# Kernel optimization log

Measured on AMD Instinct MI355X. Metric: run time of the kernel, lower is better.

## Reference

```python
import jax, jax.numpy as jnp
import numpy as np

EPS = 1e-5  # torch BatchNorm2d default eps


def _lin(x, W, b):
    # torch nn.Linear: y = x @ W.T + b, W is [out, in]
    return jnp.einsum('...i,oi->...o', x, W) + b


def _bn(x, g, b):
    # BatchNorm2d in training mode: normalize per channel (last axis here)
    # over all other axes (B, N, K) with biased variance.
    m = jnp.mean(x, axis=(0, 1, 2), keepdims=True)
    v = jnp.mean(jnp.square(x - m), axis=(0, 1, 2), keepdims=True)
    return (x - m) * jax.lax.rsqrt(v + EPS) * g + b


def _gelu(x):
    return jax.nn.gelu(x, approximate=False)  # torch F.gelu default is erf


def _knn_idx(points, k):
    # squared euclidean pairwise distances, then k smallest per query
    pn = jnp.sum(points * points, axis=-1)  # [B,N]
    d2 = pn[:, :, None] + pn[:, None, :] - 2.0 * jnp.einsum('bnd,bmd->bnm', points, points)
    _, idx = jax.lax.top_k(-d2, k)  # [B,N,k], nearest first (includes self)
    return idx


def _gather(x, idx):
    # x: [B,N,D], idx: [B,N,K] -> [B,N,K,D]
    return jax.vmap(lambda a, i: a[i])(x, idx)


def setup_inputs() -> dict:
    key = jax.random.key(0)
    ks = jax.random.split(key, 20)
    B, N, Dp, Df, k = 2, 8192, 3, 128, 16

    def lin_params(kw, kb, din, dout):
        s = 1.0 / np.sqrt(din)
        W = jax.random.uniform(kw, (dout, din), jnp.float32, -s, s)
        b = jax.random.uniform(kb, (dout,), jnp.float32, -s, s)
        return W, b

    Wq, bq = lin_params(ks[0], ks[1], Df, Df)
    Wk, bk = lin_params(ks[2], ks[3], Df, Df)
    Wv, bv = lin_params(ks[4], ks[5], Df, Df)
    Wd1, bd1 = lin_params(ks[6], ks[7], Dp, Dp)
    Wd2, bd2 = lin_params(ks[8], ks[9], Dp, Df)
    Wg1, bg1 = lin_params(ks[10], ks[11], Df, Df)
    Wg2, bg2 = lin_params(ks[12], ks[13], Df, Df)

    return {
        'feats': jax.random.normal(ks[14], (B, N, Df), jnp.float32),
        'points': jax.random.normal(ks[15], (B, N, Dp), jnp.float32),
        'Wq': Wq, 'bq': bq, 'Wk': Wk, 'bk': bk, 'Wv': Wv, 'bv': bv,
        'Wd1': Wd1, 'bd1': bd1, 'Wd2': Wd2, 'bd2': bd2,
        'Wg1': Wg1, 'bg1': bg1, 'Wg2': Wg2, 'bg2': bg2,
        'gd': jnp.ones((Dp,), jnp.float32), 'betad': jnp.zeros((Dp,), jnp.float32),
        'gg1': jnp.ones((Df,), jnp.float32), 'betag1': jnp.zeros((Df,), jnp.float32),
        'gg2': jnp.ones((Df,), jnp.float32), 'betag2': jnp.zeros((Df,), jnp.float32),
        'k': 16,
    }


def reference(feats, points, Wq, bq, Wk, bk, Wv, bv, Wd1, bd1, Wd2, bd2,
              Wg1, bg1, Wg2, bg2, gd, betad, gg1, betag1, gg2, betag2, k):
    idx = _knn_idx(points, k)                     # [B,N,k]
    knn_feats = _gather(feats, idx)               # [B,N,k,Df]
    knn_points = _gather(points, idx)             # [B,N,k,Dp]

    pos = points[:, :, None, :] - knn_points      # [B,N,k,Dp]
    pos = _lin(pos, Wd1, bd1)
    pos = _gelu(_bn(pos, gd, betad))
    pos = _lin(pos, Wd2, bd2)                     # [B,N,k,Df]

    q = _lin(feats, Wq, bq)                       # [B,N,Df]
    key_t = _lin(knn_feats, Wk, bk)               # [B,N,k,Df]
    gamma = q[:, :, None, :] - key_t + pos
    gamma = _gelu(_bn(gamma, gg1, betag1))
    gamma = _lin(gamma, Wg1, bg1)
    gamma = _gelu(_bn(gamma, gg2, betag2))
    gamma = _lin(gamma, Wg2, bg2)

    rho = jax.nn.softmax(gamma, axis=-2)          # softmax over k neighbors
    value = _lin(knn_feats, Wv, bv) + pos
    return jnp.einsum('bnkd,bnkd->bnd', rho, value)
```

## Files before the change

kernel.cpp:

```cpp
#include <hip/hip_runtime.h>
#include <hip/hip_bf16.h>
#include <math.h>

#define NPTS 8192
#define STAT_CNT 262144.0f
#define BN_EPS 1e-5f

typedef __attribute__((__ext_vector_type__(8))) __bf16 bf16x8;
typedef __attribute__((__ext_vector_type__(4))) float f32x4;

#define SD_SUM 0
#define SD_SSQ 4
#define SD_SC 8
#define SD_SH 12
#define SG1_SC 16
#define SG1_SH 144
#define SG2_SC 272
#define SG2_SH 400
#define PG1 528
#define PG2 8720
#define STATS_FLOATS 16912

__device__ __forceinline__ unsigned short f2b(float x){
  unsigned u = __float_as_uint(x);
  return (unsigned short)((u + 0x7FFFu + ((u>>16)&1u)) >> 16);
}
__device__ __forceinline__ float b2f(unsigned short h){
  return __uint_as_float(((unsigned)h)<<16);
}
__device__ __forceinline__ float gelu_f(float x){
  float u = fabsf(x)*0.70710678118654752440f;
  float t = 1.0f/fmaf(0.3275911f, u, 1.0f);
  float p = t*fmaf(t,fmaf(t,fmaf(t,fmaf(t,1.061405429f,-1.453152027f),1.421413741f),-0.284496736f),0.254829592f);
  float er = fmaf(-p, __expf(-u*u), 1.0f);
  er = (x < 0.f) ? -er : er;
  return 0.5f*x*(1.0f+er);
}
__device__ __forceinline__ int swz(int row, int byteInRow){
  return row*256 + (byteInRow ^ ((row&7)<<4));
}
__device__ __forceinline__ float dist2f(float qx,float qy,float qz,float qpn,
                                        float x,float y,float z,float w){
  return (qpn + w) - 2.0f*fmaf(qx,x,fmaf(qy,y,qz*z));
}

#define MFMA16(a,b,c) __builtin_amdgcn_mfma_f32_16x16x32_bf16((a),(b),(c),0,0,0)

__device__ __forceinline__ bf16x8 ldsA8(const unsigned short* sA, int row, int k){
  return *(const bf16x8*)((const char*)sA + swz(row, k*2));
}
__device__ __forceinline__ bf16x8 ldW8(const unsigned short* W, int n, int k){
  return *(const bf16x8*)(W + n*128 + k);
}

__device__ __forceinline__ bf16x8 bn_gelu8(uint4 raw, const float* sSC, const float* sSH, int kb0){
  union { f32x4 v[2]; float f[8]; } SC, SH;
  SC.v[0] = *(const f32x4*)&sSC[kb0]; SC.v[1] = *(const f32x4*)&sSC[kb0+4];
  SH.v[0] = *(const f32x4*)&sSH[kb0]; SH.v[1] = *(const f32x4*)&sSH[kb0+4];
  union { uint4 u; unsigned int w[4]; } U; U.u = raw;
  union { unsigned int w[4]; bf16x8 v; } O;
  #pragma unroll
  for (int p=0;p<4;++p){
    float xlo = gelu_f(fmaf(__uint_as_float(U.w[p]<<16),        SC.f[2*p],   SH.f[2*p]));
    float xhi = gelu_f(fmaf(__uint_as_float(U.w[p]&0xffff0000u), SC.f[2*p+1], SH.f[2*p+1]));
    unsigned lo = __float_as_uint(xlo), hi = __float_as_uint(xhi);
    lo = (lo + 0x7FFFu + ((lo>>16)&1u)) >> 16;
    hi = (hi + 0x7FFFu + ((hi>>16)&1u)) & 0xffff0000u;
    O.w[p] = hi | lo;
  }
  return O.v;
}

__global__ __launch_bounds__(256) void k_prep(
    const float* __restrict__ feats, const float* __restrict__ Wq, const float* __restrict__ Wk,
    const float* __restrict__ Wv, const float* __restrict__ Wg1, const float* __restrict__ Wg2,
    unsigned short* __restrict__ wbf, unsigned short* __restrict__ featb, float* __restrict__ stats)
{
  int i = blockIdx.x*256 + threadIdx.x;
  featb[i] = f2b(feats[i]);
  if (i < 16384){
    wbf[i]        = f2b(Wq[i]);
    wbf[16384+i]  = f2b(Wk[i]);
    wbf[32768+i]  = f2b(Wv[i]);
    wbf[49152+i]  = f2b(Wg1[i]);
    wbf[65536+i]  = f2b(Wg2[i]);
  }
  if (i < STATS_FLOATS) stats[i] = 0.f;
}

__global__ __launch_bounds__(256) void k_knn5(const float* __restrict__ points, int* __restrict__ idxb){
  __shared__ float svD[16][64];
  __shared__ int   svI[16][64];
  __shared__ int   svC[16];
  int tid = threadIdx.x;
  int wid = tid>>6, lane = tid&63;
  int blk = blockIdx.x;
  int b = (blk*16) >> 13;
  const float* cb = points + (size_t)b*NPTS*3;
  int qbase = blk*16 + wid*4;
  float qx[4],qy[4],qz[4],qpn[4],lmin[4],tq[4];
  #pragma unroll
  for (int q=0;q<4;++q){
    const float* qp = points + (size_t)(qbase+q)*3;
    qx[q]=qp[0]; qy[q]=qp[1]; qz[q]=qp[2];
    qpn[q]=fmaf(qz[q],qz[q],fmaf(qy[q],qy[q],qx[q]*qx[q]));
    lmin[q]=3.4e38f;
  }
  if (lane < 4) svC[wid*4+lane] = 0;
  #pragma unroll 4
  for (int s=0;s<128;++s){
    int p = s*64 + lane;
    const float* sp = cb + (size_t)p*3;
    float x=sp[0], y=sp[1], z=sp[2];
    float w = fmaf(z,z,fmaf(y,y,x*x));
    #pragma unroll
    for (int q=0;q<4;++q){
      float d = dist2f(qx[q],qy[q],qz[q],qpn[q], x,y,z,w);
      lmin[q] = fminf(lmin[q], d);
    }
  }
  #pragma unroll
  for (int q=0;q<4;++q){
    float v = lmin[q];
    #pragma unroll
    for (int k=2;k<=64;k<<=1){
      #pragma unroll
      for (int j=k>>1;j>=1;j>>=1){
        float o = __shfl_xor(v, j);
        bool keepmin = ((lane & j)==0) == ((lane & k)==0);
        v = keepmin ? fminf(v,o) : fmaxf(v,o);
      }
    }
    tq[q] = __shfl(v, 15);
  }
  #pragma unroll 2
  for (int s=0;s<128;++s){
    int p = s*64 + lane;
    const float* sp = cb + (size_t)p*3;
    float x=sp[0], y=sp[1], z=sp[2];
    float w = fmaf(z,z,fmaf(y,y,x*x));
    #pragma unroll
    for (int q=0;q<4;++q){
      float d = dist2f(qx[q],qy[q],qz[q],qpn[q], x,y,z,w);
      if (d <= tq[q]){
        int wq = wid*4+q;
        int slot = atomicAdd(&svC[wq], 1);
        if (slot < 64){ svD[wq][slot]=d; svI[wq][slot]=p; }
      }
    }
  }
  __syncthreads();
  #pragma unroll 1
  for (int q=0;q<4;++q){
    int wq = wid*4+q;
    int n = svC[wq]; n = (n>64)?64:n;
    float d = (lane<n)? svD[wq][lane] : 3.4e38f;
    int   ii = (lane<n)? svI[wq][lane] : 0x7fffffff;
    int rank = 0;
    #pragma unroll 4
    for (int j=0;j<n;++j){
      float od = svD[wq][j]; int oi = svI[wq][j];
      rank += ((od<d)||(od==d && oi<ii)) ? 1 : 0;
    }
    if (lane<n && rank<16) idxb[(size_t)(qbase+q)*16 + rank] = ii;
  }
}

__global__ __launch_bounds__(256) void k_dstats(const int* __restrict__ idxb,
    const float* __restrict__ points, const float* __restrict__ Wd1, const float* __restrict__ bd1,
    float* __restrict__ stats){
  __shared__ float sS[6];
  if (threadIdx.x < 6) sS[threadIdx.x]=0.f;
  __syncthreads();
  int qi = blockIdx.x*256 + threadIdx.x;
  int b = qi >> 13;
  const float* qp = points + (size_t)qi*3;
  float qx=qp[0],qy=qp[1],qz=qp[2];
  float w00=Wd1[0],w01=Wd1[1],w02=Wd1[2],w10=Wd1[3],w11=Wd1[4],w12=Wd1[5],w20=Wd1[6],w21=Wd1[7],w22=Wd1[8];
  float b0=bd1[0],b1=bd1[1],b2=bd1[2];
  float s0=0,s1=0,s2=0,q0=0,q1=0,q2=0;
  #pragma unroll
  for (int j=0;j<16;j++){
    int nb = idxb[(size_t)qi*16 + j];
    const float* np_ = points + (size_t)(b*NPTS + nb)*3;
    float dx=qx-np_[0], dy=qy-np_[1], dz=qz-np_[2];
    float t0 = fmaf(dz,w02,fmaf(dy,w01,dx*w00)) + b0;
    float t1 = fmaf(dz,w12,fmaf(dy,w11,dx*w10)) + b1;
    float t2 = fmaf(dz,w22,fmaf(dy,w21,dx*w20)) + b2;
    s0+=t0; s1+=t1; s2+=t2;
    q0=fmaf(t0,t0,q0); q1=fmaf(t1,t1,q1); q2=fmaf(t2,t2,q2);
  }
  atomicAdd(&sS[0],s0); atomicAdd(&sS[1],s1); atomicAdd(&sS[2],s2);
  atomicAdd(&sS[3],q0); atomicAdd(&sS[4],q1); atomicAdd(&sS[5],q2);
  __syncthreads();
  if (threadIdx.x < 3) atomicAdd(&stats[SD_SUM+threadIdx.x], sS[threadIdx.x]);
  else if (threadIdx.x < 6) atomicAdd(&stats[SD_SSQ+threadIdx.x-3], sS[threadIdx.x]);
}

__global__ void k_finalize(float* stats, int sumOff, int ssqOff, const float* __restrict__ gm,
                           const float* __restrict__ bt, int scOff, int shOff, int C){
  int c = blockIdx.x*64 + threadIdx.x;
  if (c >= C) return;
  float m = stats[sumOff+c] * (1.0f/STAT_CNT);
  float v = stats[ssqOff+c] * (1.0f/STAT_CNT) - m*m;
  v = fmaxf(v, 0.0f);
  float rs = rsqrtf(v + BN_EPS);
  float sc = gm[c]*rs;
  stats[scOff+c] = sc;
  stats[shOff+c] = fmaf(-m, sc, bt[c]);
}

__global__ void k_finalizeP(float* stats, int partOff, const float* __restrict__ gm,
                            const float* __restrict__ bt, int scOff, int shOff){
  int c = blockIdx.x*64 + threadIdx.x;
  float s=0.f, q=0.f;
  #pragma unroll 4
  for (int p=0;p<32;p++){
    s += stats[partOff + p*256 + c];
    q += stats[partOff + p*256 + 128 + c];
  }
  float m = s * (1.0f/STAT_CNT);
  float v = fmaxf(q*(1.0f/STAT_CNT) - m*m, 0.0f);
  float rs = rsqrtf(v + BN_EPS);
  float sc = gm[c]*rs;
  stats[scOff+c] = sc;
  stats[shOff+c] = fmaf(-m, sc, bt[c]);
}

__global__ __launch_bounds__(256) void k_qkv(
    const unsigned short* __restrict__ featb, const unsigned short* __restrict__ wbf,
    const float* __restrict__ bq, const float* __restrict__ bk, const float* __restrict__ bv,
    float* __restrict__ qout, unsigned short* __restrict__ kout, unsigned short* __restrict__ vout)
{
  __shared__ __align__(16) unsigned short sA[64*128];
  int tid = threadIdx.x;
  size_t row0g = (size_t)blockIdx.x*64;
  for (int t=tid; t<1024; t+=256){
    int row=t>>4, cc=t&15;
    uint4 v = *(const uint4*)(featb + (row0g+row)*128 + cc*8);
    *(uint4*)((char*)sA + swz(row, cc*16)) = v;
  }
  __syncthreads();
  int wid=tid>>6, lane=tid&63;
  int r=lane&15, g=lane>>4;
  int row0 = wid*16;
  f32x4 aQ[8]={}, aK[8]={}, aV[8]={};
  const unsigned short* WQ = wbf;
  const unsigned short* WK = wbf+16384;
  const unsigned short* WV = wbf+32768;
  #pragma unroll
  for (int ks=0;ks<4;++ks){
    int k = ks*32 + g*8;
    bf16x8 a0 = ldsA8(sA, row0+r, k);
    #pragma unroll
    for (int nt=0;nt<8;++nt){
      aQ[nt]=MFMA16(a0, ldW8(WQ,nt*16+r,k), aQ[nt]);
      aK[nt]=MFMA16(a0, ldW8(WK,nt*16+r,k), aK[nt]);
      aV[nt]=MFMA16(a0, ldW8(WV,nt*16+r,k), aV[nt]);
    }
  }
  #pragma unroll
  for (int nt=0;nt<8;++nt){
    int ch=nt*16+r;
    float bqc=bq[ch], bkc=bk[ch], bvc=bv[ch];
    #pragma unroll
    for (int rr=0;rr<4;++rr){
      size_t grow = row0g + row0 + g*4 + rr;
      qout[grow*128+ch] = aQ[nt][rr]+bqc;
      kout[grow*128+ch] = f2b(aK[nt][rr]+bkc);
      vout[grow*128+ch] = f2b(aV[nt][rr]+bvc);
    }
  }
}

__global__ __launch_bounds__(256) void k_fuse(
    const float* __restrict__ points, const int* __restrict__ idxb,
    const float* __restrict__ qbuf, const unsigned short* __restrict__ kb,
    const unsigned short* __restrict__ vb,
    const float* __restrict__ Wd1, const float* __restrict__ bd1,
    const float* __restrict__ Wd2, const float* __restrict__ bd2,
    float* __restrict__ stats,
    unsigned short* __restrict__ g1out, unsigned short* __restrict__ valout)
{
  __shared__ float sSum[128];
  __shared__ float sSq[128];
  int tid = threadIdx.x, blk = blockIdx.x;
  int slot = tid & 15, jg = tid >> 4;
  int lane = tid & 63;
  int ch0 = slot*8;
  if (tid < 128){ sSum[tid]=0.f; sSq[tid]=0.f; }
  float w2[24], b2v[8];
  #pragma unroll
  for (int u=0;u<8;++u){
    w2[u*3+0]=Wd2[(ch0+u)*3+0];
    w2[u*3+1]=Wd2[(ch0+u)*3+1];
    w2[u*3+2]=Wd2[(ch0+u)*3+2];
    b2v[u]=bd2[ch0+u];
  }
  int c = slot & 3; c = (c==3)?2:c;
  float wa  = (c==0)?Wd1[0]:((c==1)?Wd1[3]:Wd1[6]);
  float wb_ = (c==0)?Wd1[1]:((c==1)?Wd1[4]:Wd1[7]);
  float wc  = (c==0)?Wd1[2]:((c==1)?Wd1[5]:Wd1[8]);
  float bc_ = (c==0)?bd1[0]:((c==1)?bd1[1]:bd1[2]);
  float sc_ = (c==0)?stats[SD_SC+0]:((c==1)?stats[SD_SC+1]:stats[SD_SC+2]);
  float sh_ = (c==0)?stats[SD_SH+0]:((c==1)?stats[SD_SH+1]:stats[SD_SH+2]);
  int base = lane & 48;
  float accS[8]={0,0,0,0,0,0,0,0}, accQ[8]={0,0,0,0,0,0,0,0};
  __syncthreads();
  #pragma unroll 2
  for (int i=0;i<8;++i){
    int q = blk*8 + i;
    int b = q >> 13;
    int row = q*16 + jg;
    int nb = idxb[row];
    const float* ctr = points + (size_t)q*3;
    const float* np_ = points + (size_t)(b*NPTS + nb)*3;
    float dx = ctr[0]-np_[0], dy = ctr[1]-np_[1], dz = ctr[2]-np_[2];
    float t = fmaf(dz, wc, fmaf(dy, wb_, dx*wa)) + bc_;
    float tc = gelu_f(fmaf(t, sc_, sh_));
    float g0  = __shfl(tc, base+0);
    float g1v = __shfl(tc, base+1);
    float g2v = __shfl(tc, base+2);
    size_t kvoff = ((size_t)(b*NPTS + nb))*128 + ch0;
    union { uint4 u; unsigned short s[8]; } K, V, G, Vo;
    K.u = *(const uint4*)(kb + kvoff);
    V.u = *(const uint4*)(vb + kvoff);
    float4 q0 = *(const float4*)(qbuf + (size_t)q*128 + ch0);
    float4 q1 = *(const float4*)(qbuf + (size_t)q*128 + ch0 + 4);
    float qv[8] = {q0.x,q0.y,q0.z,q0.w,q1.x,q1.y,q1.z,q1.w};
    #pragma unroll
    for (int u=0;u<8;++u){
      float pos = fmaf(g2v, w2[u*3+2], fmaf(g1v, w2[u*3+1], g0*w2[u*3+0])) + b2v[u];
      float key = b2f(K.s[u]);
      float val = b2f(V.s[u]) + pos;
      float gmv = qv[u] - key + pos;
      accS[u] += gmv; accQ[u] = fmaf(gmv,gmv,accQ[u]);
      G.s[u] = f2b(gmv); Vo.s[u] = f2b(val);
    }
    *(uint4*)(g1out + (size_t)row*128 + ch0) = G.u;
    *(uint4*)(valout + (size_t)row*128 + ch0) = Vo.u;
  }
  #pragma unroll
  for (int u=0;u<8;++u){
    atomicAdd(&sSum[ch0+u], accS[u]);
    atomicAdd(&sSq[ch0+u], accQ[u]);
  }
  __syncthreads();
  if (tid < 128){
    int ps = blk & 31;
    atomicAdd(&stats[PG1 + ps*256 + tid], sSum[tid]);
    atomicAdd(&stats[PG1 + ps*256 + 128 + tid], sSq[tid]);
  }
}

__global__ __launch_bounds__(512) void k_g(
    const unsigned short* __restrict__ gin, const unsigned short* __restrict__ W,
    const float* __restrict__ bias, float* __restrict__ stats, int scOff, int shOff,
    unsigned short* __restrict__ gout, int partOff)
{
  __shared__ __align__(16) unsigned short sW[128*128];
  __shared__ float sSC[128], sSH[128];
  int tid = threadIdx.x;
  for (int t=tid; t<2048; t+=512){
    int row=t>>4, c=t&15;
    uint4 v = *(const uint4*)(W + row*128 + c*8);
    *(uint4*)((char*)sW + swz(row,c*16)) = v;
  }
  if (tid < 128){ sSC[tid]=stats[scOff+tid]; sSH[tid]=stats[shOff+tid]; }
  __syncthreads();
  int wid=tid>>6, lane=tid&63;
  int r=lane&15, g=lane>>4;
  float bs[8];
  #pragma unroll
  for (int nt=0;nt<8;++nt) bs[nt]=bias[nt*16+r];
  float accS[8]={0,0,0,0,0,0,0,0}, accQ[8]={0,0,0,0,0,0,0,0};
  for (int tile = blockIdx.x*8 + wid; tile < 16384; tile += 8192){
    size_t row0 = (size_t)tile*16;
    bf16x8 a[4];
    #pragma unroll
    for (int ks=0;ks<4;++ks){
      int kb0 = ks*32 + g*8;
      uint4 raw = *(const uint4*)(gin + (row0+r)*128 + kb0);
      a[ks] = bn_gelu8(raw, sSC, sSH, kb0);
    }
    f32x4 acc[8] = {};
    #pragma unroll
    for (int ks=0;ks<4;++ks){
      int k = ks*32 + g*8;
      #pragma unroll
      for (int nt=0;nt<8;++nt)
        acc[nt] = MFMA16(a[ks], ldsA8(sW, nt*16+r, k), acc[nt]);
    }
    #pragma unroll
    for (int nt=0;nt<8;++nt){
      #pragma unroll
      for (int rr=0;rr<4;++rr){
        float x = acc[nt][rr] + bs[nt];
        accS[nt] += x; accQ[nt] = fmaf(x,x,accQ[nt]);
        gout[(row0 + g*4 + rr)*128 + nt*16 + r] = f2b(x);
      }
    }
  }
  #pragma unroll
  for (int nt=0;nt<8;++nt){
    float s_ = accS[nt], q_ = accQ[nt];
    s_ += __shfl_xor(s_,16); s_ += __shfl_xor(s_,32);
    q_ += __shfl_xor(q_,16); q_ += __shfl_xor(q_,32);
    if (g==0){
      int slot = blockIdx.x & 31;
      atomicAdd(&stats[partOff + slot*256 + nt*16+r], s_);
      atomicAdd(&stats[partOff + slot*256 + 128 + nt*16+r], q_);
    }
  }
}

__global__ __launch_bounds__(512) void k_out(
    const unsigned short* __restrict__ gin, const unsigned short* __restrict__ W,
    const float* __restrict__ bias, const float* __restrict__ stats, int scOff, int shOff,
    const unsigned short* __restrict__ val, float* __restrict__ outp)
{
  __shared__ __align__(16) unsigned short sW[128*128];
  __shared__ float sSC[128], sSH[128];
  int tid = threadIdx.x;
  for (int t=tid; t<2048; t+=512){
    int row=t>>4, c=t&15;
    uint4 v = *(const uint4*)(W + row*128 + c*8);
    *(uint4*)((char*)sW + swz(row,c*16)) = v;
  }
  if (tid < 128){ sSC[tid]=stats[scOff+tid]; sSH[tid]=stats[shOff+tid]; }
  __syncthreads();
  int wid=tid>>6, lane=tid&63;
  int r=lane&15, g=lane>>4;
  float bs[8];
  #pragma unroll
  for (int nt=0;nt<8;++nt) bs[nt]=bias[nt*16+r];
  for (int tile = blockIdx.x*8 + wid; tile < 16384; tile += 8192){
    size_t row0 = (size_t)tile*16;
    bf16x8 a[4];
    #pragma unroll
    for (int ks=0;ks<4;++ks){
      int kb0 = ks*32 + g*8;
      uint4 raw = *(const uint4*)(gin + (row0+r)*128 + kb0);
      a[ks] = bn_gelu8(raw, sSC, sSH, kb0);
    }
    f32x4 acc[8] = {};
    #pragma unroll
    for (int ks=0;ks<4;++ks){
      int k = ks*32 + g*8;
      #pragma unroll
      for (int nt=0;nt<8;++nt)
        acc[nt] = MFMA16(a[ks], ldsA8(sW, nt*16+r, k), acc[nt]);
    }
    #pragma unroll
    for (int nt=0;nt<8;++nt){
      float g3[4];
      #pragma unroll
      for (int rr=0;rr<4;++rr) g3[rr] = acc[nt][rr] + bs[nt];
      float m = fmaxf(fmaxf(g3[0],g3[1]),fmaxf(g3[2],g3[3]));
      m = fmaxf(m, __shfl_xor(m,16));
      m = fmaxf(m, __shfl_xor(m,32));
      float s=0.f, o=0.f;
      #pragma unroll
      for (int rr=0;rr<4;++rr){
        float e = __expf(g3[rr]-m);
        float vv = b2f(val[(row0 + g*4 + rr)*128 + nt*16 + r]);
        s += e; o = fmaf(e, vv, o);
      }
      s += __shfl_xor(s,16); s += __shfl_xor(s,32);
      o += __shfl_xor(o,16); o += __shfl_xor(o,32);
      if (g==0) outp[(size_t)tile*128 + nt*16 + r] = o/s;
    }
  }
}

extern "C" void kernel_launch(void* const* d_in, const int* in_sizes, int n_in,
                              void* d_out, int out_size, void* d_ws, size_t ws_size,
                              hipStream_t stream)
{
  const float* feats  = (const float*)d_in[0];
  const float* points = (const float*)d_in[1];
  const float* Wq = (const float*)d_in[2];  const float* bq = (const float*)d_in[3];
  const float* Wk = (const float*)d_in[4];  const float* bk = (const float*)d_in[5];
  const float* Wv = (const float*)d_in[6];  const float* bv = (const float*)d_in[7];
  const float* Wd1= (const float*)d_in[8];  const float* bd1= (const float*)d_in[9];
  const float* Wd2= (const float*)d_in[10]; const float* bd2= (const float*)d_in[11];
  const float* Wg1= (const float*)d_in[12]; const float* bg1= (const float*)d_in[13];
  const float* Wg2= (const float*)d_in[14]; const float* bg2= (const float*)d_in[15];
  const float* gd = (const float*)d_in[16]; const float* betad = (const float*)d_in[17];
  const float* gg1= (const float*)d_in[18]; const float* betag1= (const float*)d_in[19];
  const float* gg2= (const float*)d_in[20]; const float* betag2= (const float*)d_in[21];
  float* outp = (float*)d_out;

  char* ws = (char*)d_ws;
  int*    idxb  = (int*)   (ws + 0);
  float*  stats = (float*) (ws + 1048576);
  unsigned short* wbf   = (unsigned short*)(ws + 1179648);
  unsigned short* featb = (unsigned short*)(ws + 1343488);
  unsigned short* kb    = (unsigned short*)(ws + 5537792);
  unsigned short* vbuf  = (unsigned short*)(ws + 9732096);
  unsigned short* g1b = (unsigned short*)(ws + 13926400);
  unsigned short* vab = (unsigned short*)(ws + 81035264);
  unsigned short* g2b = (unsigned short*)(ws + 148144128);
  float*  qbuf  = (float*) (ws + 215252992);

  k_prep<<<dim3(8192),dim3(256),0,stream>>>(feats,Wq,Wk,Wv,Wg1,Wg2,wbf,featb,stats);
  k_knn5<<<dim3(1024),dim3(256),0,stream>>>(points,idxb);
  k_dstats<<<dim3(64),dim3(256),0,stream>>>(idxb,points,Wd1,bd1,stats);
  k_finalize<<<dim3(1),dim3(64),0,stream>>>(stats,SD_SUM,SD_SSQ,gd,betad,SD_SC,SD_SH,3);
  k_qkv<<<dim3(256),dim3(256),0,stream>>>(featb,wbf,bq,bk,bv,qbuf,kb,vbuf);
  k_fuse<<<dim3(2048),dim3(256),0,stream>>>(points,idxb,qbuf,kb,vbuf,Wd1,bd1,Wd2,bd2,stats,g1b,vab);
  k_finalizeP<<<dim3(2),dim3(64),0,stream>>>(stats,PG1,gg1,betag1,SG1_SC,SG1_SH);
  k_g<<<dim3(1024),dim3(512),0,stream>>>(g1b,wbf+49152,bg1,stats,SG1_SC,SG1_SH,g2b,PG2);
  k_finalizeP<<<dim3(2),dim3(64),0,stream>>>(stats,PG2,gg2,betag2,SG2_SC,SG2_SH);
  k_out<<<dim3(1024),dim3(512),0,stream>>>(g2b,wbf+65536,bg2,stats,SG2_SC,SG2_SH,vab,outp);
  (void)in_sizes; (void)n_in; (void)out_size; (void)ws_size;
}
```

Before: 348.5 us.

## Stage k_g and k_out global traffic through LDS for coalesced 16-byte accesses

In k_g, the per-lane scattered bf16 output stores are replaced by writes into a per-wave swizzled LDS tile. The tile is then written out as coalesced 16-byte chunks. In k_out, the value tile is first loaded into LDS with 16-byte loads and the softmax-weighted outputs are gathered in LDS before one float2 store per lane. The grid is halved so each block processes four tiles per wave, amortizing the weight load into LDS. This adds about 32KB of LDS per block, which may reduce occupancy.

After: 421.8 us. +21.0%, slower.

```diff
diff --git a/kernel.cpp b/kernel.cpp
--- a/kernel.cpp
+++ b/kernel.cpp
@@ -360,6 +360,7 @@
 {
   __shared__ __align__(16) unsigned short sW[128*128];
   __shared__ float sSC[128], sSH[128];
+  __shared__ __align__(16) unsigned short sOut[8][2048];
   int tid = threadIdx.x;
   for (int t=tid; t<2048; t+=512){
     int row=t>>4, c=t&15;
@@ -370,11 +371,14 @@
   __syncthreads();
   int wid=tid>>6, lane=tid&63;
   int r=lane&15, g=lane>>4;
+  unsigned short* myOut = sOut[wid];
   float bs[8];
   #pragma unroll
   for (int nt=0;nt<8;++nt) bs[nt]=bias[nt*16+r];
   float accS[8]={0,0,0,0,0,0,0,0}, accQ[8]={0,0,0,0,0,0,0,0};
-  for (int tile = blockIdx.x*8 + wid; tile < 16384; tile += 8192){
+  #pragma unroll 1
+  for (int t2=0; t2<4; ++t2){
+    int tile = blockIdx.x*8 + wid + t2*4096;
     size_t row0 = (size_t)tile*16;
     bf16x8 a[4];
     #pragma unroll
@@ -397,8 +401,15 @@
       for (int rr=0;rr<4;++rr){
         float x = acc[nt][rr] + bs[nt];
         accS[nt] += x; accQ[nt] = fmaf(x,x,accQ[nt]);
-        gout[(row0 + g*4 + rr)*128 + nt*16 + r] = f2b(x);
+        *(unsigned short*)((char*)myOut + swz(g*4+rr, (nt*16+r)*2)) = f2b(x);
       }
+    }
+    #pragma unroll
+    for (int j=0;j<4;++j){
+      int cch = j*64 + lane;
+      int row = cch>>4, ci = cch&15;
+      uint4 v = *(const uint4*)((const char*)myOut + swz(row, ci*16));
+      *(uint4*)(gout + (row0 + row)*128 + ci*8) = v;
     }
   }
   #pragma unroll
@@ -421,6 +432,8 @@
 {
   __shared__ __align__(16) unsigned short sW[128*128];
   __shared__ float sSC[128], sSH[128];
+  __shared__ __align__(16) unsigned short sVal[8][2048];
+  __shared__ float sO[8][128];
   int tid = threadIdx.x;
   for (int t=tid; t<2048; t+=512){
     int row=t>>4, c=t&15;
@@ -431,11 +444,21 @@
   __syncthreads();
   int wid=tid>>6, lane=tid&63;
   int r=lane&15, g=lane>>4;
+  unsigned short* myVal = sVal[wid];
+  float* myO = sO[wid];
   float bs[8];
   #pragma unroll
   for (int nt=0;nt<8;++nt) bs[nt]=bias[nt*16+r];
-  for (int tile = blockIdx.x*8 + wid; tile < 16384; tile += 8192){
+  #pragma unroll 1
+  for (int t2=0; t2<4; ++t2){
+    int tile = blockIdx.x*8 + wid + t2*4096;
     size_t row0 = (size_t)tile*16;
+    #pragma unroll
+    for (int ks=0;ks<4;++ks){
+      int kb0 = ks*32 + g*8;
+      uint4 vv = *(const uint4*)(val + (row0+r)*128 + kb0);
+      *(uint4*)((char*)myVal + swz(r, kb0*2)) = vv;
+    }
     bf16x8 a[4];
     #pragma unroll
     for (int ks=0;ks<4;++ks){
@@ -463,13 +486,15 @@
       #pragma unroll
       for (int rr=0;rr<4;++rr){
         float e = __expf(g3[rr]-m);
-        float vv = b2f(val[(row0 + g*4 + rr)*128 + nt*16 + r]);
+        float vv = b2f(*(const unsigned short*)((const char*)myVal + swz(g*4+rr, (nt*16+r)*2)));
         s += e; o = fmaf(e, vv, o);
       }
       s += __shfl_xor(s,16); s += __shfl_xor(s,32);
       o += __shfl_xor(o,16); o += __shfl_xor(o,32);
-      if (g==0) outp[(size_t)tile*128 + nt*16 + r] = o/s;
-    }
+      if (g==0) myO[nt*16+r] = o/s;
+    }
+    float2 ov = *(const float2*)&myO[lane*2];
+    *(float2*)(outp + (size_t)tile*128 + lane*2) = ov;
   }
 }
 
@@ -510,8 +535,8 @@
   k_qkv<<<dim3(256),dim3(256),0,stream>>>(featb,wbf,bq,bk,bv,qbuf,kb,vbuf);
   k_fuse<<<dim3(2048),dim3(256),0,stream>>>(points,idxb,qbuf,kb,vbuf,Wd1,bd1,Wd2,bd2,stats,g1b,vab);
   k_finalizeP<<<dim3(2),dim3(64),0,stream>>>(stats,PG1,gg1,betag1,SG1_SC,SG1_SH);
-  k_g<<<dim3(1024),dim3(512),0,stream>>>(g1b,wbf+49152,bg1,stats,SG1_SC,SG1_SH,g2b,PG2);
+  k_g<<<dim3(512),dim3(512),0,stream>>>(g1b,wbf+49152,bg1,stats,SG1_SC,SG1_SH,g2b,PG2);
   k_finalizeP<<<dim3(2),dim3(64),0,stream>>>(stats,PG2,gg2,betag2,SG2_SC,SG2_SH);
-  k_out<<<dim3(1024),dim3(512),0,stream>>>(g2b,wbf+65536,bg2,stats,SG2_SC,SG2_SH,vab,outp);
+  k_out<<<dim3(512),dim3(512),0,stream>>>(g2b,wbf+65536,bg2,stats,SG2_SC,SG2_SH,vab,outp);
   (void)in_sizes; (void)n_in; (void)out_size; (void)ws_size;
 }
```
